# Performance work log

Hardware: AMD Instinct MI355X
Metric: run time of the kernel (lower is better)

The kernel has to match this reference:

```python
import jax, jax.numpy as jnp
import numpy as np
from jax import lax

C = 256
POOL = 7
NUM_CLASSES = 81
D = NUM_CLASSES - 1
STRIDES = (4, 8, 16, 32)
DEC_MULT = (0.1, 0.1, 0.2, 0.2)  # decode_settings: multipliers on raw deltas
LOG_MAX = float(np.log(1000.0 / 16.0))


def setup_inputs() -> dict:
    key = jax.random.key(0)
    ks = jax.random.split(key, 16)
    n, Rp = 2, 512
    R = n * Rp
    img = 800.0
    cx = jax.random.uniform(ks[0], (R,), minval=0.0, maxval=img)
    cy = jax.random.uniform(ks[1], (R,), minval=0.0, maxval=img)
    w = jax.random.uniform(ks[2], (R,), minval=16.0, maxval=300.0)
    h = jax.random.uniform(ks[3], (R,), minval=16.0, maxval=300.0)
    x1 = jnp.clip(cx - w / 2, 0.0, img - 1.0)
    y1 = jnp.clip(cy - h / 2, 0.0, img - 1.0)
    x2 = jnp.minimum(jnp.maximum(cx + w / 2, x1 + 1.0), img)
    y2 = jnp.minimum(jnp.maximum(cy + h / 2, y1 + 1.0), img)
    proposals = jnp.stack([x1, y1, x2, y2], -1)
    imidx = jnp.repeat(jnp.arange(n, dtype=jnp.int32), Rp)
    fmaps = {}
    for li, s in enumerate(STRIDES):
        hw = int(800 // s)
        fmaps[f"fmap{li}"] = jax.random.normal(ks[4 + li], (n, hw, hw, C), jnp.float32)
    c1, clin = C * POOL * POOL, 1024
    def lin(k, fi, fo):
        return (jax.random.normal(k, (fi, fo), jnp.float32) / np.sqrt(fi).astype(np.float32),
                jnp.zeros((fo,), jnp.float32))
    W0, b0 = lin(ks[8], c1, clin)
    W1, b1 = lin(ks[9], clin, clin)
    Wc, bc = lin(ks[10], clin, NUM_CLASSES)
    Wr, br = lin(ks[11], clin, NUM_CLASSES * 4)
    imsizes = jnp.full((n, 2), img, jnp.float32)  # (h, w) per image
    return dict(proposals=proposals, imidx=imidx, **fmaps,
                W0=W0, b0=b0, W1=W1, b1=b1, Wc=Wc, bc=bc, Wr=Wr, br=br,
                imsizes=imsizes, score_thr=0.05, iou_thr=0.5, imtop=100, min_size=1.0)


def _roi_align_level(fmap, boxes, imidx, stride):
    # fmap [n,H,W,C], boxes [R,4] xyxy in image coords; 1 sample per bin, bilinear.
    n, H, W, c = fmap.shape
    s = 1.0 / stride
    x1, y1, x2, y2 = boxes[:, 0] * s, boxes[:, 1] * s, boxes[:, 2] * s, boxes[:, 3] * s
    g = (jnp.arange(POOL, dtype=jnp.float32) + 0.5) / POOL  # bin centers in [0,1]
    xs = x1[:, None] + g[None, :] * (x2 - x1)[:, None] - 0.5  # [R,POOL]
    ys = y1[:, None] + g[None, :] * (y2 - y1)[:, None] - 0.5
    R = boxes.shape[0]
    xx = jnp.broadcast_to(xs[:, None, :], (R, POOL, POOL))
    yy = jnp.broadcast_to(ys[:, :, None], (R, POOL, POOL))
    x0f, y0f = jnp.floor(xx), jnp.floor(yy)
    wx, wy = xx - x0f, yy - y0f
    x0 = jnp.clip(x0f.astype(jnp.int32), 0, W - 1)
    x1i = jnp.clip(x0f.astype(jnp.int32) + 1, 0, W - 1)
    y0 = jnp.clip(y0f.astype(jnp.int32), 0, H - 1)
    y1i = jnp.clip(y0f.astype(jnp.int32) + 1, 0, H - 1)
    ii = imidx[:, None, None]
    v00 = fmap[ii, y0, x0]; v01 = fmap[ii, y0, x1i]
    v10 = fmap[ii, y1i, x0]; v11 = fmap[ii, y1i, x1i]  # each [R,POOL,POOL,C]
    wx, wy = wx[..., None], wy[..., None]
    return (v00 * (1 - wx) * (1 - wy) + v01 * wx * (1 - wy)
            + v10 * (1 - wx) * wy + v11 * wx * wy)


def _forward(proposals, imidx, fmaps, W0, b0, W1, b1, Wc, bc, Wr, br,
             imsizes, score_thr, iou_thr, imtop, min_size):
    R = proposals.shape[0]
    pw = proposals[:, 2] - proposals[:, 0]
    ph = proposals[:, 3] - proposals[:, 1]
    # FPN level assignment (torchvision canonical formula)
    lvl = jnp.floor(4.0 + jnp.log2(jnp.sqrt(pw * ph) / 224.0 + 1e-6))
    lvl = jnp.clip(lvl, 2, 5).astype(jnp.int32) - 2
    pooled = jnp.zeros((R, POOL, POOL, C), fmaps[0].dtype)
    for k, (fm, st) in enumerate(zip(fmaps, STRIDES)):
        pk = _roi_align_level(fm, proposals, imidx, st)
        pooled = jnp.where((lvl == k)[:, None, None, None], pk, pooled)
    # two-FC head + cls/reg
    x = pooled.reshape(R, -1)
    x = jax.nn.relu(x @ W0 + b0)
    x = jax.nn.relu(x @ W1 + b1)
    reg = (x @ Wr + br).reshape(R, NUM_CLASSES, 4)[:, 1:]      # [R,D,4]
    scr = jax.nn.softmax(x @ Wc + bc, axis=-1)[:, 1:]          # [R,D]
    cls = jnp.broadcast_to(jnp.arange(1, NUM_CLASSES, dtype=jnp.int32), (R, D))
    # decode boxes (proposal cwh + weighted deltas, log-space clamp)
    cx = (proposals[:, 0] + proposals[:, 2]) * 0.5
    cy = (proposals[:, 1] + proposals[:, 3]) * 0.5
    dx = reg[..., 0] * DEC_MULT[0]
    dy = reg[..., 1] * DEC_MULT[1]
    dw = jnp.minimum(reg[..., 2] * DEC_MULT[2], LOG_MAX)
    dh = jnp.minimum(reg[..., 3] * DEC_MULT[3], LOG_MAX)
    ncx = dx * pw[:, None] + cx[:, None]
    ncy = dy * ph[:, None] + cy[:, None]
    nw = jnp.exp(dw) * pw[:, None]
    nh = jnp.exp(dh) * ph[:, None]
    hb = imsizes[imidx, 0][:, None]
    wb = imsizes[imidx, 1][:, None]
    bx1 = jnp.clip(ncx - nw / 2, 0.0, wb); bx2 = jnp.clip(ncx + nw / 2, 0.0, wb)
    by1 = jnp.clip(ncy - nh / 2, 0.0, hb); by2 = jnp.clip(ncy + nh / 2, 0.0, hb)
    boxes = jnp.stack([bx1, by1, bx2, by2], -1)                # [R,D,4]
    valid = (scr > score_thr) & (bx2 - bx1 >= min_size) & (by2 - by1 >= min_size)
    # flatten roi-class pairs; class-offset boxes = torchvision batched_nms trick
    M = R * D
    boxes_f = boxes.reshape(M, 4)
    scr_f = scr.reshape(M)
    cls_f = cls.reshape(M)
    valid_f = valid.reshape(M)
    imidx_f = jnp.repeat(imidx, D)
    off = cls_f.astype(boxes_f.dtype)[:, None] * (jnp.max(imsizes) + 2.0)
    bo = boxes_f + off
    areas = (bo[:, 2] - bo[:, 0]) * (bo[:, 3] - bo[:, 1])
    def nms(scores0):
        def step(scores, _):
            i = jnp.argmax(scores)
            s = scores[i]
            b = bo[i]
            iw = jnp.clip(jnp.minimum(b[2], bo[:, 2]) - jnp.maximum(b[0], bo[:, 0]), 0.0)
            ih = jnp.clip(jnp.minimum(b[3], bo[:, 3]) - jnp.maximum(b[1], bo[:, 1]), 0.0)
            inter = iw * ih
            iou = inter / (areas[i] + areas - inter + 1e-6)
            scores = jnp.where(iou > iou_thr, -1.0, scores)
            scores = scores.at[i].set(-1.0)
            return scores, (i, s)
        _, (idx, s) = lax.scan(step, scores0, None, length=imtop)
        return idx, s
    n = imsizes.shape[0]
    ob, osc, ocl = [], [], []
    for i in range(n):
        s0 = jnp.where(valid_f & (imidx_f == i), scr_f, -1.0)
        idx, s = nms(s0)
        keep = s > 0.0  # padded slots have score <= 0
        ob.append(jnp.where(keep[:, None], boxes_f[idx], 0.0))
        osc.append(jnp.where(keep, s, 0.0))
        ocl.append(jnp.where(keep, cls_f[idx], -1))
    return jnp.stack(ob), jnp.stack(osc), jnp.stack(ocl)


def reference(proposals, imidx, fmap0, fmap1, fmap2, fmap3, W0, b0, W1, b1,
              Wc, bc, Wr, br, imsizes, score_thr, iou_thr, imtop, min_size):
    return _forward(proposals, imidx, (fmap0, fmap1, fmap2, fmap3), W0, b0, W1,
                    b1, Wc, bc, Wr, br, imsizes, score_thr, iou_thr, int(imtop),
                    min_size)
```

## Files before the change

### kernel.cpp

```cpp
#include <hip/hip_runtime.h>
#include <math.h>

#define CCH 256
#define NPOOL 7
#define NCLS 81
#define DCLS 80
#define NHEAD 512
#define FLOG_MAX 4.1351666f

typedef _Float16 half8 __attribute__((ext_vector_type(8)));
typedef _Float16 half4 __attribute__((ext_vector_type(4)));
typedef float floatx4 __attribute__((ext_vector_type(4)));

__global__ void zero_k(float4* __restrict__ p, int count4)
{
    int i = blockIdx.x * blockDim.x + threadIdx.x;
    if (i < count4) p[i] = make_float4(0.f, 0.f, 0.f, 0.f);
}

__device__ __forceinline__ void roi_setup(
    const float* __restrict__ prop, const int* __restrict__ imidx,
    const float* __restrict__ f0, const float* __restrict__ f1,
    const float* __restrict__ f2, const float* __restrict__ f3,
    int h0, int h1, int h2, int h3, int b,
// ... 9 lines not shown

    float lv = floorf(4.0f + log2f(sqrtf(pw * ph) / 224.0f + 1e-6f));
    lv = fminf(fmaxf(lv, 2.0f), 5.0f);
    int lvl = (int)lv - 2;

    const float* fm; int H; float s;
    if (lvl == 0)      { fm = f0; H = h0; s = 0.25f;    }
    else if (lvl == 1) { fm = f1; H = h1; s = 0.125f;   }
    else if (lvl == 2) { fm = f2; H = h2; s = 0.0625f;  }
    else               { fm = f3; H = h3; s = 0.03125f; }
    W = H;

    float xs1 = x1 * s, ys1 = y1 * s, xs2 = x2 * s, ys2 = y2 * s;
    float gx = (px + 0.5f) / 7.0f, gy = (py + 0.5f) / 7.0f;
    float xx = xs1 + gx * (xs2 - xs1) - 0.5f;
    float yy = ys1 + gy * (ys2 - ys1) - 0.5f;
    float x0f = floorf(xx), y0f = floorf(yy);
    float wx = xx - x0f, wy = yy - y0f;
    int x0i = min(max((int)x0f, 0), W - 1);
    int x1i = min(max((int)x0f + 1, 0), W - 1);
    int y0i = min(max((int)y0f, 0), H - 1);
    int y1i = min(max((int)y0f + 1, 0), H - 1);

    int ii = imidx[roi];
    base = fm + (size_t)ii * H * W * CCH;
    o00 = ((size_t)y0i * W + x0i) * CCH;
    o01 = ((size_t)y0i * W + x1i) * CCH;
    o10 = ((size_t)y1i * W + x0i) * CCH;
    o11 = ((size_t)y1i * W + x1i) * CCH;
    w00 = (1.0f - wx) * (1.0f - wy);
    w01 = wx * (1.0f - wy);
    w10 = (1.0f - wx) * wy;
    w11 = wx * wy;
}

__global__ void roi_align_k(const float* __restrict__ prop,
                            const int* __restrict__ imidx,
                            const float* __restrict__ f0,
                            const float* __restrict__ f1,
                            const float* __restrict__ f2,
                            const float* __restrict__ f3,
                            int h0, int h1, int h2, int h3,
                            float* __restrict__ pooled)
{
    int b = blockIdx.x, c = threadIdx.x;
    const float* base; int W; size_t o00, o01, o10, o11;
    float w00, w01, w10, w11;
    roi_setup(prop, imidx, f0, f1, f2, f3, h0, h1, h2, h3, b,
              base, W, o00, o01, o10, o11, w00, w01, w10, w11);
    float v = base[o00 + c] * w00 + base[o01 + c] * w01
            + base[o10 + c] * w10 + base[o11 + c] * w11;
    pooled[(size_t)b * CCH + c] = v;
}


__device__ __forceinline__ void roi_f16v4_body(
    const float* __restrict__ prop, const int* __restrict__ imidx,
    const float* __restrict__ f0, const float* __restrict__ f1,
    const float* __restrict__ f2, const float* __restrict__ f3,
    int h0, int h1, int h2, int h3, int bb, int t,
    _Float16* __restrict__ poolH, _Float16* __restrict__ poolL)
{
    int b = bb * 4 + (t >> 6);
    int lane = t & 63;
    const float* base; int W; size_t o00, o01, o10, o11;
    float w00, w01, w10, w11;
    roi_setup(prop, imidx, f0, f1, f2, f3, h0, h1, h2, h3, b,
              base, W, o00, o01, o10, o11, w00, w01, w10, w11);

    int c4 = lane * 4;
    float4 v00 = *(const float4*)(base + o00 + c4);
    float4 v01 = *(const float4*)(base + o01 + c4);
    float4 v10 = *(const float4*)(base + o10 + c4);
    float4 v11 = *(const float4*)(base + o11 + c4);
    const float* p00 = (const float*)&v00;
    const float* p01 = (const float*)&v01;
    const float* p10 = (const float*)&v10;
    const float* p11 = (const float*)&v11;

    half4 h, l;
#pragma unroll
    for (int e = 0; e < 4; ++e) {
        float v = p00[e] * w00 + p01[e] * w01 + p10[e] * w10 + p11[e] * w11;
        _Float16 hh = (_Float16)v;
        h[e] = hh;
        l[e] = (_Float16)(v - (float)hh);
    }
    size_t idx = (size_t)b * CCH + c4;
    *(half4*)(poolH + idx) = h;
    *(half4*)(poolL + idx) = l;
}

__device__ __forceinline__ void conv_fast_body(
    const float* __restrict__ W, _Float16* __restrict__ WtH,
    _Float16* __restrict__ WtL, int K, int N, int k0, int n0, int t,
    float (*sh)[65])
{
#pragma unroll
    for (int p = 0; p < 4; ++p) {
        int idx = p * 256 + t;
        int kr = idx >> 4, nc = (idx & 15) * 4;
        float4 v = *(const float4*)(W + (size_t)(k0 + kr) * N + n0 + nc);
        sh[kr][nc + 0] = v.x; sh[kr][nc + 1] = v.y;
        sh[kr][nc + 2] = v.z; sh[kr][nc + 3] = v.w;
    }
    __syncthreads();
#pragma unroll
// ... 9 lines not shown
            l[i] = (_Float16)(v - (float)hh);
        }
        *(half4*)(WtH + (size_t)(n0 + nr) * K + k0 + kc) = h;
        *(half4*)(WtL + (size_t)(n0 + nr) * K + k0 + kc) = l;
    }
}

__device__ __forceinline__ void conv_guard_body(
    const float* __restrict__ W, _Float16* __restrict__ WtH,
    _Float16* __restrict__ WtL, int K, int N, int Kt, int rowofs,
    int k0, int n0, int t, float (*sh)[65])
{
#pragma unroll
    for (int p = 0; p < 4; ++p) {
        int idx = p * 256 + t;
        int kr = idx >> 4, nc = (idx & 15) * 4;
#pragma unroll
        for (int e = 0; e < 4; ++e) {
            int nn = n0 + nc + e;
            sh[kr][nc + e] = (nn < N) ? W[(size_t)(k0 + kr) * N + nn] : 0.0f;
        }
    }
    __syncthreads();
#pragma unroll
    for (int p = 0; p < 4; ++p) {
        int idx = p * 256 + t;
        int nr = idx >> 4, kc = (idx & 15) * 4;
        if (n0 + nr < N) {
            half4 h, l;
#pragma unroll
            for (int i = 0; i < 4; ++i) {
                float v = sh[kc + i][nr];
                _Float16 hh = (_Float16)v;
                h[i] = hh;
                l[i] = (_Float16)(v - (float)hh);
            }
            *(half4*)(WtH + (size_t)(rowofs + n0 + nr) * Kt + k0 + kc) = h;
            *(half4*)(WtL + (size_t)(rowofs + n0 + nr) * Kt + k0 + kc) = l;
        }
    }
}

__global__ __launch_bounds__(256) void pre_uber_k(
    const float* __restrict__ prop, const int* __restrict__ imidx,
    const float* __restrict__ f0, const float* __restrict__ f1,
    const float* __restrict__ f2, const float* __restrict__ f3,
    int h0, int h1, int h2, int h3,
    _Float16* __restrict__ poolH, _Float16* __restrict__ poolL,
    const float* __restrict__ W0, _Float16* __restrict__ W0tH, _Float16* __restrict__ W0tL,
    const float* __restrict__ W1, _Float16* __restrict__ W1tH, _Float16* __restrict__ W1tL,
    const float* __restrict__ Wc, const float* __restrict__ Wr,
    _Float16* __restrict__ WheadtH, _Float16* __restrict__ WheadtL,
    float4* __restrict__ zp, int zc4,
    int R, int K0, int CL)
{
    __shared__ float sh[64][65];
    int b = blockIdx.x, t = threadIdx.x;

    int NB_ROI = (R * 49) / 4;
    int KT0 = K0 / 64, NT0 = CL / 64;
    int NB_CW0 = KT0 * NT0;
    int KT1 = CL / 64;
    int NB_CW1 = KT1 * KT1;
    int NTc = (NCLS + 63) / 64;
    int NB_CWc = KT1 * NTc;
    int NTr = (NCLS * 4 + 63) / 64;
    int NB_CWr = KT1 * NTr;

    if (b < NB_ROI) {
        roi_f16v4_body(prop, imidx, f0, f1, f2, f3, h0, h1, h2, h3, b, t,
                       poolH, poolL);
        return;
    }
    b -= NB_ROI;
    if (b < NB_CW0) {
        int k0 = (b % KT0) * 64, n0 = (b / KT0) * 64;
        conv_fast_body(W0, W0tH, W0tL, K0, CL, k0, n0, t, sh);
        return;
    }
    b -= NB_CW0;
    if (b < NB_CW1) {
        int k0 = (b % KT1) * 64, n0 = (b / KT1) * 64;
        conv_fast_body(W1, W1tH, W1tL, CL, CL, k0, n0, t, sh);
        return;
    }
    b -= NB_CW1;
    if (b < NB_CWc) {
        int k0 = (b % KT1) * 64, n0 = (b / KT1) * 64;
        conv_guard_body(Wc, WheadtH, WheadtL, CL, NCLS, CL, 0, k0, n0, t, sh);
        return;
    }
    b -= NB_CWc;
    if (b < NB_CWr) {
        int k0 = (b % KT1) * 64, n0 = (b / KT1) * 64;
        conv_guard_body(Wr, WheadtH, WheadtL, CL, NCLS * 4, CL, NCLS, k0, n0, t, sh);
        return;
    }
    b -= NB_CWr;
    {
        int i = b * 256 + t;
        if (i < zc4) zp[i] = make_float4(0.f, 0.f, 0.f, 0.f);
    }
}

__global__ __launch_bounds__(256) void convert_w_t_k(const float* __restrict__ W,
                                                     _Float16* __restrict__ WtH,
                                                     _Float16* __restrict__ WtL,
                                                     int K, int N)
{
    __shared__ float sh[64][65];
    conv_fast_body(W, WtH, WtL, K, N, blockIdx.x * 64, blockIdx.y * 64,
                   threadIdx.x, sh);
}

__global__ __launch_bounds__(256) void convert_w_t_guard_k(const float* __restrict__ W,
                                                           _Float16* __restrict__ WtH,
                                                           _Float16* __restrict__ WtL,
                                                           int K, int N, int Kt, int rowofs)
{
    __shared__ float sh[64][65];
    conv_guard_body(W, WtH, WtL, K, N, Kt, rowofs, blockIdx.x * 64,
                    blockIdx.y * 64, threadIdx.x, sh);
}

__global__ void act_split_k(const float* __restrict__ acc,
                            const float* __restrict__ bias,
                            _Float16* __restrict__ outH,
                            _Float16* __restrict__ outL,
                            int total, int CL)
{
    int i = (blockIdx.x * blockDim.x + threadIdx.x) * 4;
    if (i >= total) return;
    int b = i % CL;
    float4 v = *(const float4*)(acc + i);
    float4 bb = *(const float4*)(bias + b);
    const float* pv = (const float*)&v;
    const float* pb = (const float*)&bb;
    half4 h, l;
#pragma unroll
    for (int e = 0; e < 4; ++e) {
        float f = fmaxf(pv[e] + pb[e], 0.0f);
        _Float16 hh = (_Float16)f;
        h[e] = hh;
        l[e] = (_Float16)(f - (float)hh);
    }
    *(half4*)(outH + i) = h;
    *(half4*)(outL + i) = l;
}

__device__ __forceinline__ void dma16(const _Float16* g, _Float16* l)
{
    __builtin_amdgcn_global_load_lds(
        (const __attribute__((address_space(1))) unsigned int*)g,
        (__attribute__((address_space(3))) unsigned int*)l, 16, 0, 0);
}

#define LDKE 32
#define DKQ_SWZ(lane)  ((((lane) & 3) ^ (((lane) >> 3) & 3)) << 3)
#define FK_SWZ(lane)   (((((lane) >> 4) ^ (((lane) >> 1) & 3))) << 3)

__global__ __launch_bounds__(256) void gemm_mfma_split_k(
    const _Float16* __restrict__ Ah, const _Float16* __restrict__ Al,
    const _Float16* __restrict__ Bh, const _Float16* __restrict__ Bl,
    float* __restrict__ Cacc, int M, int N, int K, int Kc, int SP)
{
    __shared__ _Float16 sAh[128 * LDKE], sAl[128 * LDKE];
    __shared__ _Float16 sBh[128 * LDKE], sBl[128 * LDKE];

    int bid = blockIdx.x;
    int z = bid % SP;
    int q = bid / SP;
    int NT = N >> 7;
    int nn = q % NT;
    int m = q / NT;
    int m0 = m * 128, n0 = nn * 128;
    int kb = z * Kc;
    int ke = min(K, kb + Kc);

    int t = threadIdx.x;
    int lane = t & 63, w = t >> 6;
    int wr = w >> 1, wc = w & 1;
    int fr = lane & 15;
    int fk = FK_SWZ(lane);

    int drow = w * 32 + (lane >> 2);
    int dkq = DKQ_SWZ(lane);
    const _Float16* gAh = Ah + (size_t)(m0 + drow) * K + dkq;
    const _Float16* gAl = Al + (size_t)(m0 + drow) * K + dkq;
    const _Float16* gBh = Bh + (size_t)(n0 + drow) * K + dkq;
    const _Float16* gBl = Bl + (size_t)(n0 + drow) * K + dkq;
    size_t rowskip = (size_t)16 * K;

    _Float16* lAh0 = &sAh[(w * 2 + 0) * 512];
    _Float16* lAh1 = &sAh[(w * 2 + 1) * 512];
    _Float16* lAl0 = &sAl[(w * 2 + 0) * 512];
    _Float16* lAl1 = &sAl[(w * 2 + 1) * 512];
    _Float16* lBh0 = &sBh[(w * 2 + 0) * 512];
    _Float16* lBh1 = &sBh[(w * 2 + 1) * 512];
    _Float16* lBl0 = &sBl[(w * 2 + 0) * 512];
    _Float16* lBl1 = &sBl[(w * 2 + 1) * 512];

    floatx4 acc[4][4] = {};

    for (int k0 = kb; k0 < ke; k0 += 32) {
        dma16(gAh + k0, lAh0);
        dma16(gAh + rowskip + k0, lAh1);
        dma16(gAl + k0, lAl0);
        dma16(gAl + rowskip + k0, lAl1);
        dma16(gBh + k0, lBh0);
        dma16(gBh + rowskip + k0, lBh1);
        dma16(gBl + k0, lBl0);
        dma16(gBl + rowskip + k0, lBl1);
        __syncthreads();

        half8 ah[4], al[4], bh[4], bl[4];
#pragma unroll
        for (int i = 0; i < 4; ++i) {
            int ar = wr * 64 + i * 16 + fr;
            ah[i] = *(const half8*)&sAh[ar * LDKE + fk];
            al[i] = *(const half8*)&sAl[ar * LDKE + fk];
            int bc = wc * 64 + i * 16 + fr;
            bh[i] = *(const half8*)&sBh[bc * LDKE + fk];
            bl[i] = *(const half8*)&sBl[bc * LDKE + fk];
        }
#pragma unroll
        for (int i = 0; i < 4; ++i)
#pragma unroll
            for (int j = 0; j < 4; ++j) {
                acc[i][j] = __builtin_amdgcn_mfma_f32_16x16x32_f16(ah[i], bh[j], acc[i][j], 0, 0, 0);
                acc[i][j] = __builtin_amdgcn_mfma_f32_16x16x32_f16(ah[i], bl[j], acc[i][j], 0, 0, 0);
                acc[i][j] = __builtin_amdgcn_mfma_f32_16x16x32_f16(al[i], bh[j], acc[i][j], 0, 0, 0);
            }
        __syncthreads();
    }

    int rbase = (lane >> 4) * 4;
#pragma unroll
    for (int i = 0; i < 4; ++i)
#pragma unroll
        for (int j = 0; j < 4; ++j) {
            int col = n0 + wc * 64 + j * 16 + fr;
#pragma unroll
            for (int r = 0; r < 4; ++r) {
                int row = m0 + wr * 64 + i * 16 + rbase + r;
                atomicAdd(&Cacc[(size_t)row * N + col], acc[i][j][r]);
            }
        }
}

__global__ __launch_bounds__(256) void gemm_mfma_fused64_k(
    const _Float16* __restrict__ Ah, const _Float16* __restrict__ Al,
    const _Float16* __restrict__ Bh, const _Float16* __restrict__ Bl,
    const float* __restrict__ bias,
    float* __restrict__ Cout,
    _Float16* __restrict__ outH, _Float16* __restrict__ outL,
    int M, int N, int K, int mode)
{
    __shared__ _Float16 sAh[2][64 * LDKE], sAl[2][64 * LDKE];
    __shared__ _Float16 sBh[2][64 * LDKE], sBl[2][64 * LDKE];

    int m0 = blockIdx.y * 64, n0 = blockIdx.x * 64;
    int t = threadIdx.x;
    int lane = t & 63, w = t >> 6;
    int wr = w >> 1, wc = w & 1;
    int fr = lane & 15;
    int fk = FK_SWZ(lane);

    int drow = w * 16 + (lane >> 2);
    int dkq = DKQ_SWZ(lane);
    const _Float16* gAh = Ah + (size_t)(m0 + drow) * K + dkq;
    const _Float16* gAl = Al + (size_t)(m0 + drow) * K + dkq;
    const _Float16* gBh = Bh + (size_t)(n0 + drow) * K + dkq;
    const _Float16* gBl = Bl + (size_t)(n0 + drow) * K + dkq;
    int lofs = w * 512;

    int nt = K >> 5;

    dma16(gAh + 0, &sAh[0][lofs]);
    dma16(gAl + 0, &sAl[0][lofs]);
    dma16(gBh + 0, &sBh[0][lofs]);
    dma16(gBl + 0, &sBl[0][lofs]);
    __syncthreads();

    floatx4 acc[2][2] = {};

    for (int tt = 0; tt < nt; ++tt) {
        int c = tt & 1, nb = c ^ 1;
        if (tt + 1 < nt) {
            int k1 = (tt + 1) << 5;
            dma16(gAh + k1, &sAh[nb][lofs]);
            dma16(gAl + k1, &sAl[nb][lofs]);
            dma16(gBh + k1, &sBh[nb][lofs]);
            dma16(gBl + k1, &sBl[nb][lofs]);
        }
// ... 93 lines not shown

#pragma unroll
        for (int kk = 0; kk < 16; ++kk) {
            float4 af = *(const float4*)&Ast[kk][ty * 4];
            float4 bf = *(const float4*)&Bs[kk][tx * 4];
            float a_[4] = {af.x, af.y, af.z, af.w};
            float b_[4] = {bf.x, bf.y, bf.z, bf.w};
#pragma unroll
            for (int i = 0; i < 4; ++i)
#pragma unroll
                for (int j = 0; j < 4; ++j)
                    acc[i][j] = fmaf(a_[i], b_[j], acc[i][j]);
        }
    }

#pragma unroll
    for (int i = 0; i < 4; ++i) {
        int row = m0 + ty * 4 + i;
#pragma unroll
        for (int j = 0; j < 4; ++j) {
            int col = n0 + tx * 4 + j;
            if (col < N) atomicAdd(&Cacc[(size_t)row * N + col], acc[i][j]);
        }
    }
}

__global__ void softmax_k(const float* __restrict__ logits, int ldl,
                          const float* __restrict__ bc,
                          float* __restrict__ scr)
{
    int r = blockIdx.x;
    int t = threadIdx.x;
    const float* row = logits + (size_t)r * ldl;

    float v0 = row[t] + bc[t];
    float v1 = (t + 64 < NCLS) ? (row[t + 64] + bc[t + 64]) : -INFINITY;
    float m = fmaxf(v0, v1);
#pragma unroll
    for (int o = 32; o > 0; o >>= 1) m = fmaxf(m, __shfl_down(m, o));
    m = __shfl(m, 0);

    float e0 = expf(v0 - m);
    float e1 = (t + 64 < NCLS) ? expf(v1 - m) : 0.0f;
    float sum = e0 + e1;
#pragma unroll
    for (int o = 32; o > 0; o >>= 1) sum += __shfl_down(sum, o);
    sum = __shfl(sum, 0);
    float inv = 1.0f / sum;

    if (t >= 1)        scr[(size_t)r * DCLS + (t - 1)]  = e0 * inv;
    if (t + 64 < NCLS) scr[(size_t)r * DCLS + (t + 63)] = e1 * inv;
}

#define NMS_T 1024
#define NMS_SORTMAX 4096
#define NMS_AMAX 512
__global__ __launch_bounds__(NMS_T) void nms_k(
    const float* __restrict__ scr,
    const float* __restrict__ prop,
    const int* __restrict__ imidx,
    const float* __restrict__ head, int ldh, int regofs,
    const float* __restrict__ br,
    const float* __restrict__ imsz,
    const float* __restrict__ score_thr_p,
    const float* __restrict__ min_size_p,
    const float* __restrict__ iou_thr_p,
    int* __restrict__ cidx,
    float* __restrict__ cscore,
    float* __restrict__ cbo,
    float* __restrict__ cbox,
    float* __restrict__ carea,
    float* __restrict__ out,
    int M, int n, int imtop)
{
    int img = blockIdx.x;
    int t = threadIdx.x;
    const int T = NMS_T;
    const int NW = NMS_T / 64;
    int lane = t & 63, wid = t >> 6;

    __shared__ int cnt;
    __shared__ unsigned long long skey[NMS_SORTMAX];
    __shared__ int sp_[NMS_SORTMAX];
    __shared__ float aab0[NMS_AMAX], aab1[NMS_AMAX], aab2[NMS_AMAX], aab3[NMS_AMAX], aaa[NMS_AMAX];
    __shared__ int f_it;
    __shared__ float ws_sc[NW];
    __shared__ int ws_g[NW], ws_p[NW];
    __shared__ float f_sc, f_o0, f_o1, f_o2, f_o3, f_ar;

    if (t == 0) cnt = 0;
    __syncthreads();

    float score_thr = score_thr_p[0];
    float min_size  = min_size_p[0];
    float iou_thr   = iou_thr_p[0];
    float immax = imsz[0];
    for (int q = 1; q < 2 * n; ++q) immax = fmaxf(immax, imsz[q]);

    int base = img * M;
    for (int j = t; j < M; j += T) {
        int r = j / DCLS;
        if (imidx[r] != img) continue;
        float s = scr[j];
        if (s <= score_thr) continue;

        int cls = j - r * DCLS + 1;
        const float* pr = prop + (size_t)r * 4;
        float pw = pr[2] - pr[0], ph = pr[3] - pr[1];
        float cx = (pr[0] + pr[2]) * 0.5f, cy = (pr[1] + pr[3]) * 0.5f;
        const float* rg_ = head + (size_t)r * ldh + regofs + cls * 4;
        const float* bb = br + cls * 4;
        float dx = (rg_[0] + bb[0]) * 0.1f;
        float dy = (rg_[1] + bb[1]) * 0.1f;
        float dw = fminf((rg_[2] + bb[2]) * 0.2f, FLOG_MAX);
        float dh = fminf((rg_[3] + bb[3]) * 0.2f, FLOG_MAX);
        float ncx = dx * pw + cx;
        float ncy = dy * ph + cy;
        float nw = expf(dw) * pw;
        float nh = expf(dh) * ph;
        float hbound = imsz[img * 2 + 0];
        float wbound = imsz[img * 2 + 1];
        float bx1 = fminf(fmaxf(ncx - nw * 0.5f, 0.0f), wbound);
        float bx2 = fminf(fmaxf(ncx + nw * 0.5f, 0.0f), wbound);
        float by1 = fminf(fmaxf(ncy - nh * 0.5f, 0.0f), hbound);
        float by2 = fminf(fmaxf(ncy + nh * 0.5f, 0.0f), hbound);
        if (bx2 - bx1 < min_size || by2 - by1 < min_size) continue;

        float off = (float)cls * (immax + 2.0f);
        int p = atomicAdd(&cnt, 1);
        cidx[base + p] = j;
        cscore[base + p] = s;
        cbox[(size_t)(base + p) * 4 + 0] = bx1;
        cbox[(size_t)(base + p) * 4 + 1] = by1;
        cbox[(size_t)(base + p) * 4 + 2] = bx2;
        cbox[(size_t)(base + p) * 4 + 3] = by2;
        cbo[(size_t)(base + p) * 4 + 0] = bx1 + off;
        cbo[(size_t)(base + p) * 4 + 1] = by1 + off;
        cbo[(size_t)(base + p) * 4 + 2] = bx2 + off;
        cbo[(size_t)(base + p) * 4 + 3] = by2 + off;
        carea[base + p] = (bx2 - bx1) * (by2 - by1);
    }
    __syncthreads();
    int K = cnt;

    float* ob  = out;
    float* osc = out + (size_t)n * imtop * 4;
    float* ocl = out + (size_t)n * imtop * 5;

    int it = 0;
    if (K <= NMS_SORTMAX && imtop <= NMS_AMAX) {
        int SN = 64; while (SN < K) SN <<= 1;
        for (int i = t; i < SN; i += T) {
            if (i < K) {
                unsigned int sb = __float_as_uint(cscore[base + i]);
                skey[i] = ((unsigned long long)sb << 32)
                        | (unsigned int)(~cidx[base + i]);
            } else {
                skey[i] = 0ull;
            }
            sp_[i] = i;
        }
        for (int k = 2; k <= SN; k <<= 1) {
            for (int j = k >> 1; j > 0; j >>= 1) {
                __syncthreads();
                for (int i = t; i < SN; i += T) {
                    int l = i ^ j;
                    if (l > i) {
                        unsigned long long ki = skey[i], kl = skey[l];
                        bool up = ((i & k) == 0);
                        bool sw = up ? (ki < kl) : (ki > kl);
                        if (sw) {
                            skey[i] = kl; skey[l] = ki;
                            int tp = sp_[i]; sp_[i] = sp_[l]; sp_[l] = tp;
                        }
                    }
                }
            }
        }
        __syncthreads();

        if (wid == 0) {
            int na = 0;
            for (int c0 = 0; c0 < K && na < imtop; c0 += 64) {
                int ci = c0 + lane;
                bool alive = ci < K;
                float x0 = 0.f, x1 = 0.f, x2 = 0.f, x3 = 0.f, ar_ = 0.f, sc = 0.f;
                float q0 = 0.f, q1 = 0.f, q2 = 0.f, q3 = 0.f;
                int g = 0;
                if (alive) {
                    unsigned long long key = skey[ci];
                    sc = __uint_as_float((unsigned int)(key >> 32));
                    int pp = sp_[ci];
                    g = cidx[base + pp];
                    x0 = cbo[(size_t)(base + pp) * 4 + 0];
                    x1 = cbo[(size_t)(base + pp) * 4 + 1];
                    x2 = cbo[(size_t)(base + pp) * 4 + 2];
// ... 73 lines not shown
                    int   ol = __shfl_down(l2, o);
                    if (os > b2 || (os == b2 && og < g2)) { b2 = os; g2 = og; l2 = ol; }
                }
                if (lane == 0) {
                    f_sc = b2;
                    if (b2 > 0.0f) {
                        int lp = l2;
                        size_t oslot = (size_t)img * imtop + it;
                        ob[oslot * 4 + 0] = cbox[(size_t)(base + lp) * 4 + 0];
                        ob[oslot * 4 + 1] = cbox[(size_t)(base + lp) * 4 + 1];
                        ob[oslot * 4 + 2] = cbox[(size_t)(base + lp) * 4 + 2];
                        ob[oslot * 4 + 3] = cbox[(size_t)(base + lp) * 4 + 3];
                        osc[oslot] = b2;
                        ocl[oslot] = (float)(g2 % DCLS + 1);
                        f_o0 = cbo[(size_t)(base + lp) * 4 + 0];
                        f_o1 = cbo[(size_t)(base + lp) * 4 + 1];
                        f_o2 = cbo[(size_t)(base + lp) * 4 + 2];
                        f_o3 = cbo[(size_t)(base + lp) * 4 + 3];
                        f_ar = carea[base + lp];
                        cscore[base + lp] = -1.0f;
                    }
                }
            }
            __syncthreads();
            if (f_sc <= 0.0f) break;

            float b0 = f_o0, b1 = f_o1, b2_ = f_o2, b3 = f_o3, ai = f_ar;
            for (int p = t; p < K; p += T) {
                float c0 = cbo[(size_t)(base + p) * 4 + 0];
                float c1 = cbo[(size_t)(base + p) * 4 + 1];
                float c2 = cbo[(size_t)(base + p) * 4 + 2];
                float c3 = cbo[(size_t)(base + p) * 4 + 3];
                float iw = fmaxf(fminf(b2_, c2) - fmaxf(b0, c0), 0.0f);
                float ih = fmaxf(fminf(b3, c3) - fmaxf(b1, c1), 0.0f);
                float inter = iw * ih;
                float iou = inter / (ai + carea[base + p] - inter + 1e-6f);
                if (iou > iou_thr) cscore[base + p] = -1.0f;
            }
            __syncthreads();
        }
    }

    for (int q = it + t; q < imtop; q += T) {
        size_t oslot = (size_t)img * imtop + q;
        ob[oslot * 4 + 0] = 0.0f;
        ob[oslot * 4 + 1] = 0.0f;
        ob[oslot * 4 + 2] = 0.0f;
        ob[oslot * 4 + 3] = 0.0f;
        osc[oslot] = 0.0f;
        ocl[oslot] = -1.0f;
    }
}

extern "C" void kernel_launch(void* const* d_in, const int* in_sizes, int n_in,
                              void* d_out, int out_size, void* d_ws, size_t ws_size,
                              hipStream_t stream)
{
    const float* prop   = (const float*)d_in[0];
    const int*   imidx  = (const int*)d_in[1];
    const float* f0     = (const float*)d_in[2];
    const float* f1     = (const float*)d_in[3];
    const float* f2     = (const float*)d_in[4];
    const float* f3     = (const float*)d_in[5];
    const float* W0     = (const float*)d_in[6];
    const float* b0     = (const float*)d_in[7];
    const float* W1     = (const float*)d_in[8];
    const float* b1     = (const float*)d_in[9];
    const float* Wc     = (const float*)d_in[10];
    const float* bc     = (const float*)d_in[11];
    const float* Wr     = (const float*)d_in[12];
    const float* br     = (const float*)d_in[13];
    const float* imsz   = (const float*)d_in[14];
    const float* sthr   = (const float*)d_in[15];
    const float* ithr   = (const float*)d_in[16];
    const float* msz    = (const float*)d_in[18];

    int R = in_sizes[1];
    int n = in_sizes[14] / 2;
    int imtop = out_size / (n * 6);
    int M = R * DCLS;
    int K0 = NPOOL * NPOOL * CCH;
    int CL = in_sizes[7];

    int h0 = (int)(sqrtf((float)(in_sizes[2] / (n * CCH))) + 0.5f);
    int h1 = (int)(sqrtf((float)(in_sizes[3] / (n * CCH))) + 0.5f);
    int h2 = (int)(sqrtf((float)(in_sizes[4] / (n * CCH))) + 0.5f);
    int h3 = (int)(sqrtf((float)(in_sizes[5] / (n * CCH))) + 0.5f);

    float* outf = (float*)d_out;

    size_t szPool  = (size_t)R * K0 * 2;
    size_t szX     = (size_t)R * CL * 4;
    size_t szHead  = (size_t)R * NHEAD * 4;
    size_t szWh    = (size_t)NHEAD * CL * 2;
    size_t szXh    = (size_t)R * CL * 2;
    size_t szW1t   = (size_t)CL * CL * 2;
    size_t szScr   = (size_t)R * DCLS * 4;

    size_t needed = 4 * szPool + 2 * szX + szHead + 2 * szWh
                  + 4 * szXh + 2 * szW1t + szScr;

    int splitK0 = 8;
    bool mfma_ok = (ws_size >= needed) && (R % 128 == 0) && (CL % 128 == 0)
                 && (K0 % (splitK0 * 32) == 0) && (CL % 32 == 0)
                 && ((R * 49) % 4 == 0) && (K0 % 64 == 0) && (CL % 64 == 0);

    if (mfma_ok) {
        uint8_t* w = (uint8_t*)d_ws;
        size_t o = 0;
        _Float16* poolH   = (_Float16*)(w + o); o += szPool;
        _Float16* poolL   = (_Float16*)(w + o); o += szPool;
        _Float16* W0tH    = (_Float16*)(w + o); o += szPool;
        _Float16* W0tL    = (_Float16*)(w + o); o += szPool;
        float*    x0acc   = (float*)(w + o);    o += szX;
        float*    unused  = (float*)(w + o);    o += szX;
        float*    headacc = (float*)(w + o);    o += szHead;
        _Float16* WheadtH = (_Float16*)(w + o); o += szWh;
        _Float16* WheadtL = (_Float16*)(w + o); o += szWh;
        _Float16* x0H     = (_Float16*)(w + o); o += szXh;
        _Float16* x0L     = (_Float16*)(w + o); o += szXh;
        _Float16* x1H     = (_Float16*)(w + o); o += szXh;
        _Float16* x1L     = (_Float16*)(w + o); o += szXh;
        _Float16* W1tH    = (_Float16*)(w + o); o += szW1t;
        _Float16* W1tL    = (_Float16*)(w + o); o += szW1t;
        float*    scr     = (float*)(w + o);
        (void)unused;

        int*   cidx   = (int*)d_ws;
        float* cscore = (float*)(cidx + (size_t)n * M);
        float* cbo    = cscore + (size_t)n * M;
        float* cbox   = cbo + (size_t)n * M * 4;
        float* carea  = cbox + (size_t)n * M * 4;

        {
            int NB_ROI = (R * 49) / 4;
            int NB_CW0 = (K0 / 64) * (CL / 64);
            int NB_CW1 = (CL / 64) * (CL / 64);
            int NB_CWc = (CL / 64) * ((NCLS + 63) / 64);
            int NB_CWr = (CL / 64) * ((NCLS * 4 + 63) / 64);
            int zc4    = (int)(szX / 16);
            int NB_Z   = (zc4 + 255) / 256;
            int NB = NB_ROI + NB_CW0 + NB_CW1 + NB_CWc + NB_CWr + NB_Z;
            pre_uber_k<<<dim3(NB), dim3(256), 0, stream>>>(
                prop, imidx, f0, f1, f2, f3, h0, h1, h2, h3,
                poolH, poolL,
                W0, W0tH, W0tL,
                W1, W1tH, W1tL,
                Wc, Wr, WheadtH, WheadtL,
                (float4*)x0acc, zc4,
                R, K0, CL);
        }
        gemm_mfma_split_k<<<dim3(splitK0 * (R / 128) * (CL / 128)), dim3(256), 0, stream>>>(
            poolH, poolL, W0tH, W0tL, x0acc, R, CL, K0, K0 / splitK0, splitK0);
        act_split_k<<<dim3((R * CL / 4 + 255) / 256), dim3(256), 0, stream>>>(
            x0acc, b0, x0H, x0L, R * CL, CL);
        gemm_mfma_fused64_k<<<dim3(CL / 64, R / 64), dim3(256), 0, stream>>>(
            x0H, x0L, W1tH, W1tL, b1, nullptr, x1H, x1L, R, CL, CL, 1);
        gemm_mfma_fused64_k<<<dim3(NHEAD / 64, R / 64), dim3(256), 0, stream>>>(
            x1H, x1L, WheadtH, WheadtL, nullptr, headacc, nullptr, nullptr, R, NHEAD, CL, 0);
        softmax_k<<<dim3(R), dim3(64), 0, stream>>>(headacc, NHEAD, bc, scr);
        nms_k<<<dim3(n), dim3(NMS_T), 0, stream>>>(
            scr, prop, imidx, headacc, NHEAD, NCLS, br, imsz, sthr, msz, ithr,
            cidx, cscore, cbo, cbox, carea, outf, M, n, imtop);
    } else {
        float* ws = (float*)d_ws;
        size_t off = 0;
        float* pooled  = ws + off; off += (size_t)R * K0;
        float* x0acc   = ws + off; off += (size_t)R * CL;
        float* x1acc   = ws + off; off += (size_t)R * CL;
        float* logits  = ws + off; off += (size_t)R * NCLS;
        off = (off + 3) & ~(size_t)3;
        float* reg     = ws + off; off += (size_t)R * NCLS * 4;
        float* scr     = ws + off; off += (size_t)R * DCLS;

        int*   cidx   = (int*)ws;
        float* cscore = (float*)(cidx + (size_t)n * M);
        float* cbo    = cscore + (size_t)n * M;
        float* cbox   = cbo + (size_t)n * M * 4;
        float* carea  = cbox + (size_t)n * M * 4;

        {
            size_t zcount = (size_t)(reg + (size_t)R * NCLS * 4 - x0acc);
            int c4 = (int)(zcount / 4);
            zero_k<<<dim3((c4 + 255) / 256), dim3(256), 0, stream>>>((float4*)x0acc, c4);
        }
        roi_align_k<<<dim3(R * 49), dim3(256), 0, stream>>>(
            prop, imidx, f0, f1, f2, f3, h0, h1, h2, h3, pooled);
        gemm_splitk_k<<<dim3(CL / 64, R / 64, 8), dim3(256), 0, stream>>>(
            pooled, W0, nullptr, x0acc, R, CL, K0, 1568);
        gemm_splitk_k<<<dim3(CL / 64, R / 64, 4), dim3(256), 0, stream>>>(
            x0acc, W1, b0, x1acc, R, CL, CL, 256);
        gemm_splitk_k<<<dim3((NCLS + 63) / 64, R / 64, 8), dim3(256), 0, stream>>>(
            x1acc, Wc, b1, logits, R, NCLS, CL, 128);
        gemm_splitk_k<<<dim3((NCLS * 4 + 63) / 64, R / 64, 4), dim3(256), 0, stream>>>(
            x1acc, Wr, b1, reg, R, NCLS * 4, CL, 256);
        softmax_k<<<dim3(R), dim3(64), 0, stream>>>(logits, NCLS, bc, scr);
        nms_k<<<dim3(n), dim3(NMS_T), 0, stream>>>(
            scr, prop, imidx, reg, NCLS * 4, 0, br, imsz, sthr, msz, ithr,
            cidx, cscore, cbo, cbox, carea, outf, M, n, imtop);
    }
}
```

Before: 401.9 us.

## Split NMS compaction into parallel kernel fused with softmax; narrow split-K GEMM tile

```diff
diff --git a/kernel.cpp b/kernel.cpp
--- a/kernel.cpp
+++ b/kernel.cpp
@@ -85,7 +85,6 @@
             + base[o10 + c] * w10 + base[o11 + c] * w11;
     pooled[(size_t)b * CCH + c] = v;
 }
-
 
 __device__ __forceinline__ void roi_f16v4_body(
     const float* __restrict__ prop, const int* __restrict__ imidx,
@@ -201,10 +200,13 @@
     const float* __restrict__ Wc, const float* __restrict__ Wr,
     _Float16* __restrict__ WheadtH, _Float16* __restrict__ WheadtL,
     float4* __restrict__ zp, int zc4,
+    int* __restrict__ cntp, int ncnt,
     int R, int K0, int CL)
 {
     __shared__ float sh[64][65];
     int b = blockIdx.x, t = threadIdx.x;
+
+    if (blockIdx.x == 0 && t < ncnt) cntp[t] = 0;
 
     int NB_ROI = (R * 49) / 4;
     int KT0 = K0 / 64, NT0 = CL / 64;
@@ -252,26 +254,6 @@
     }
 }
 
-__global__ __launch_bounds__(256) void convert_w_t_k(const float* __restrict__ W,
-                                                     _Float16* __restrict__ WtH,
-                                                     _Float16* __restrict__ WtL,
-                                                     int K, int N)
-{
-    __shared__ float sh[64][65];
-    conv_fast_body(W, WtH, WtL, K, N, blockIdx.x * 64, blockIdx.y * 64,
-                   threadIdx.x, sh);
-}
-
-__global__ __launch_bounds__(256) void convert_w_t_guard_k(const float* __restrict__ W,
-                                                           _Float16* __restrict__ WtH,
-                                                           _Float16* __restrict__ WtL,
-                                                           int K, int N, int Kt, int rowofs)
-{
-    __shared__ float sh[64][65];
-    conv_guard_body(W, WtH, WtL, K, N, Kt, rowofs, blockIdx.x * 64,
-                    blockIdx.y * 64, threadIdx.x, sh);
-}
-
 __global__ void act_split_k(const float* __restrict__ acc,
                             const float* __restrict__ bias,
                             _Float16* __restrict__ outH,
@@ -314,15 +296,15 @@
     float* __restrict__ Cacc, int M, int N, int K, int Kc, int SP)
 {
     __shared__ _Float16 sAh[128 * LDKE], sAl[128 * LDKE];
-    __shared__ _Float16 sBh[128 * LDKE], sBl[128 * LDKE];
+    __shared__ _Float16 sBh[64 * LDKE],  sBl[64 * LDKE];
 
     int bid = blockIdx.x;
     int z = bid % SP;
     int q = bid / SP;
-    int NT = N >> 7;
+    int NT = N >> 6;
     int nn = q % NT;
     int m = q / NT;
-    int m0 = m * 128, n0 = nn * 128;
+    int m0 = m * 128, n0 = nn * 64;
     int kb = z * Kc;
     int ke = min(K, kb + Kc);
 
@@ -332,50 +314,50 @@
     int fr = lane & 15;
     int fk = FK_SWZ(lane);
 
-    int drow = w * 32 + (lane >> 2);
+    int drowA = w * 32 + (lane >> 2);
+    int drowB = w * 16 + (lane >> 2);
     int dkq = DKQ_SWZ(lane);
-    const _Float16* gAh = Ah + (size_t)(m0 + drow) * K + dkq;
-    const _Float16* gAl = Al + (size_t)(m0 + drow) * K + dkq;
-    const _Float16* gBh = Bh + (size_t)(n0 + drow) * K + dkq;
-    const _Float16* gBl = Bl + (size_t)(n0 + drow) * K + dkq;
+    const _Float16* gAh = Ah + (size_t)(m0 + drowA) * K + dkq;
+    const _Float16* gAl = Al + (size_t)(m0 + drowA) * K + dkq;
+    const _Float16* gBh = Bh + (size_t)(n0 + drowB) * K + dkq;
+    const _Float16* gBl = Bl + (size_t)(n0 + drowB) * K + dkq;
     size_t rowskip = (size_t)16 * K;
 
     _Float16* lAh0 = &sAh[(w * 2 + 0) * 512];
     _Float16* lAh1 = &sAh[(w * 2 + 1) * 512];
     _Float16* lAl0 = &sAl[(w * 2 + 0) * 512];
     _Float16* lAl1 = &sAl[(w * 2 + 1) * 512];
-    _Float16* lBh0 = &sBh[(w * 2 + 0) * 512];
-    _Float16* lBh1 = &sBh[(w * 2 + 1) * 512];
-    _Float16* lBl0 = &sBl[(w * 2 + 0) * 512];
-    _Float16* lBl1 = &sBl[(w * 2 + 1) * 512];
-
-    floatx4 acc[4][4] = {};
+    _Float16* lBh  = &sBh[w * 512];
+    _Float16* lBl  = &sBl[w * 512];
+
+    floatx4 acc[4][2] = {};
 
     for (int k0 = kb; k0 < ke; k0 += 32) {
         dma16(gAh + k0, lAh0);
         dma16(gAh + rowskip + k0, lAh1);
         dma16(gAl + k0, lAl0);
         dma16(gAl + rowskip + k0, lAl1);
-        dma16(gBh + k0, lBh0);
-        dma16(gBh + rowskip + k0, lBh1);
-        dma16(gBl + k0, lBl0);
-        dma16(gBl + rowskip + k0, lBl1);
+        dma16(gBh + k0, lBh);
+        dma16(gBl + k0, lBl);
         __syncthreads();
 
-        half8 ah[4], al[4], bh[4], bl[4];
+        half8 ah[4], al[4], bh[2], bl[2];
 #pragma unroll
         for (int i = 0; i < 4; ++i) {
             int ar = wr * 64 + i * 16 + fr;
             ah[i] = *(const half8*)&sAh[ar * LDKE + fk];
             al[i] = *(const half8*)&sAl[ar * LDKE + fk];
-            int bc = wc * 64 + i * 16 + fr;
-            bh[i] = *(const half8*)&sBh[bc * LDKE + fk];
-            bl[i] = *(const half8*)&sBl[bc * LDKE + fk];
+        }
+#pragma unroll
+        for (int j = 0; j < 2; ++j) {
+            int bcc = wc * 32 + j * 16 + fr;
+            bh[j] = *(const half8*)&sBh[bcc * LDKE + fk];
+            bl[j] = *(const half8*)&sBl[bcc * LDKE + fk];
         }
 #pragma unroll
         for (int i = 0; i < 4; ++i)
 #pragma unroll
-            for (int j = 0; j < 4; ++j) {
+            for (int j = 0; j < 2; ++j) {
                 acc[i][j] = __builtin_amdgcn_mfma_f32_16x16x32_f16(ah[i], bh[j], acc[i][j], 0, 0, 0);
                 acc[i][j] = __builtin_amdgcn_mfma_f32_16x16x32_f16(ah[i], bl[j], acc[i][j], 0, 0, 0);
                 acc[i][j] = __builtin_amdgcn_mfma_f32_16x16x32_f16(al[i], bh[j], acc[i][j], 0, 0, 0);
@@ -387,8 +369,8 @@
 #pragma unroll
     for (int i = 0; i < 4; ++i)
 #pragma unroll
-        for (int j = 0; j < 4; ++j) {
-            int col = n0 + wc * 64 + j * 16 + fr;
+        for (int j = 0; j < 2; ++j) {
+            int col = n0 + wc * 32 + j * 16 + fr;
 #pragma unroll
             for (int r = 0; r < 4; ++r) {
                 int row = m0 + wr * 64 + i * 16 + rbase + r;
@@ -588,62 +570,63 @@
     if (t + 64 < NCLS) scr[(size_t)r * DCLS + (t + 63)] = e1 * inv;
 }
 
-#define NMS_T 1024
-#define NMS_SORTMAX 4096
-#define NMS_AMAX 512
-__global__ __launch_bounds__(NMS_T) void nms_k(
-    const float* __restrict__ scr,
+__global__ __launch_bounds__(256) void compact_k(
+    const float* __restrict__ head, int ldh, int regofs,
+    const float* __restrict__ bc,
+    const float* __restrict__ br,
     const float* __restrict__ prop,
     const int* __restrict__ imidx,
-    const float* __restrict__ head, int ldh, int regofs,
-    const float* __restrict__ br,
     const float* __restrict__ imsz,
     const float* __restrict__ score_thr_p,
     const float* __restrict__ min_size_p,
-    const float* __restrict__ iou_thr_p,
+    int* __restrict__ cntp,
     int* __restrict__ cidx,
     float* __restrict__ cscore,
     float* __restrict__ cbo,
     float* __restrict__ cbox,
     float* __restrict__ carea,
-    float* __restrict__ out,
-    int M, int n, int imtop)
-{
-    int img = blockIdx.x;
-    int t = threadIdx.x;
-    const int T = NMS_T;
-    const int NW = NMS_T / 64;
-    int lane = t & 63, wid = t >> 6;
-
-    __shared__ int cnt;
-    __shared__ unsigned long long skey[NMS_SORTMAX];
-    __shared__ int sp_[NMS_SORTMAX];
-    __shared__ float aab0[NMS_AMAX], aab1[NMS_AMAX], aab2[NMS_AMAX], aab3[NMS_AMAX], aaa[NMS_AMAX];
-    __shared__ int f_it;
-    __shared__ float ws_sc[NW];
-    __shared__ int ws_g[NW], ws_p[NW];
-    __shared__ float f_sc, f_o0, f_o1, f_o2, f_o3, f_ar;
-
-    if (t == 0) cnt = 0;
-    __syncthreads();
+    int M, int n, int R)
+{
+    int wid = threadIdx.x >> 6, t = threadIdx.x & 63;
+    int r = blockIdx.x * 4 + wid;
+    if (r >= R) return;
+
+    const float* row = head + (size_t)r * ldh;
+    float v0 = row[t] + bc[t];
+    float v1 = (t + 64 < NCLS) ? (row[t + 64] + bc[t + 64]) : -INFINITY;
+    float m = fmaxf(v0, v1);
+#pragma unroll
+    for (int o = 32; o > 0; o >>= 1) m = fmaxf(m, __shfl_down(m, o));
+    m = __shfl(m, 0);
+
+    float e0 = expf(v0 - m);
+    float e1 = (t + 64 < NCLS) ? expf(v1 - m) : 0.0f;
+    float sum = e0 + e1;
+#pragma unroll
+    for (int o = 32; o > 0; o >>= 1) sum += __shfl_down(sum, o);
+    sum = __shfl(sum, 0);
+    float inv = 1.0f / sum;
 
     float score_thr = score_thr_p[0];
     float min_size  = min_size_p[0];
-    float iou_thr   = iou_thr_p[0];
     float immax = imsz[0];
     for (int q = 1; q < 2 * n; ++q) immax = fmaxf(immax, imsz[q]);
 
+    int img = imidx[r];
     int base = img * M;
-    for (int j = t; j < M; j += T) {
-        int r = j / DCLS;
-        if (imidx[r] != img) continue;
-        float s = scr[j];
-        if (s <= score_thr) continue;
-
-        int cls = j - r * DCLS + 1;
-        const float* pr = prop + (size_t)r * 4;
-        float pw = pr[2] - pr[0], ph = pr[3] - pr[1];
-        float cx = (pr[0] + pr[2]) * 0.5f, cy = (pr[1] + pr[3]) * 0.5f;
+    const float* pr = prop + (size_t)r * 4;
+    float pw = pr[2] - pr[0], ph = pr[3] - pr[1];
+    float cx = (pr[0] + pr[2]) * 0.5f, cy = (pr[1] + pr[3]) * 0.5f;
+    float hbound = imsz[img * 2 + 0];
+    float wbound = imsz[img * 2 + 1];
+
+#pragma unroll
+    for (int pass = 0; pass < 2; ++pass) {
+        int cls; float s; bool active;
+        if (pass == 0) { cls = t;      s = e0 * inv; active = (t >= 1); }
+        else           { cls = t + 64; s = e1 * inv; active = (t + 64 < NCLS); }
+        if (!active || s <= score_thr) continue;
+
         const float* rg_ = head + (size_t)r * ldh + regofs + cls * 4;
         const float* bb = br + cls * 4;
         float dx = (rg_[0] + bb[0]) * 0.1f;
@@ -654,8 +637,6 @@
         float ncy = dy * ph + cy;
         float nw = expf(dw) * pw;
         float nh = expf(dh) * ph;
-        float hbound = imsz[img * 2 + 0];
-        float wbound = imsz[img * 2 + 1];
         float bx1 = fminf(fmaxf(ncx - nw * 0.5f, 0.0f), wbound);
         float bx2 = fminf(fmaxf(ncx + nw * 0.5f, 0.0f), wbound);
         float by1 = fminf(fmaxf(ncy - nh * 0.5f, 0.0f), hbound);
@@ -663,7 +644,8 @@
         if (bx2 - bx1 < min_size || by2 - by1 < min_size) continue;
 
         float off = (float)cls * (immax + 2.0f);
-        int p = atomicAdd(&cnt, 1);
+        int j = r * DCLS + cls - 1;
+        int p = atomicAdd(&cntp[img], 1);
         cidx[base + p] = j;
         cscore[base + p] = s;
         cbox[(size_t)(base + p) * 4 + 0] = bx1;
@@ -676,8 +658,39 @@
         cbo[(size_t)(base + p) * 4 + 3] = by2 + off;
         carea[base + p] = (bx2 - bx1) * (by2 - by1);
     }
-    __syncthreads();
-    int K = cnt;
+}
+
+#define NMS_T 1024
+#define NMS_SORTMAX 4096
+#define NMS_AMAX 512
+__global__ __launch_bounds__(NMS_T) void nms_pick_k(
+    const float* __restrict__ iou_thr_p,
+    const int* __restrict__ cntp,
+    int* __restrict__ cidx,
+    float* __restrict__ cscore,
+    float* __restrict__ cbo,
+    float* __restrict__ cbox,
+    float* __restrict__ carea,
+    float* __restrict__ out,
+    int M, int n, int imtop)
+{
+    int img = blockIdx.x;
+    int t = threadIdx.x;
+    const int T = NMS_T;
+    const int NW = NMS_T / 64;
+    int lane = t & 63, wid = t >> 6;
+
+    __shared__ unsigned long long skey[NMS_SORTMAX];
+    __shared__ int sp_[NMS_SORTMAX];
+    __shared__ float aab0[NMS_AMAX], aab1[NMS_AMAX], aab2[NMS_AMAX], aab3[NMS_AMAX], aaa[NMS_AMAX];
+    __shared__ int f_it;
+    __shared__ float ws_sc[NW];
+    __shared__ int ws_g[NW], ws_p[NW];
+    __shared__ float f_sc, f_o0, f_o1, f_o2, f_o3, f_ar;
+
+    float iou_thr = iou_thr_p[0];
+    int K = cntp[img];
+    int base = img * M;
 
     float* ob  = out;
     float* osc = out + (size_t)n * imtop * 4;
@@ -857,6 +870,171 @@
     }
 }
 
+__global__ __launch_bounds__(NMS_T) void nms_k(
+    const float* __restrict__ scr,
+    const float* __restrict__ prop,
+    const int* __restrict__ imidx,
+    const float* __restrict__ head, int ldh, int regofs,
+    const float* __restrict__ br,
+    const float* __restrict__ imsz,
+    const float* __restrict__ score_thr_p,
+    const float* __restrict__ min_size_p,
+    const float* __restrict__ iou_thr_p,
+    int* __restrict__ cidx,
+    float* __restrict__ cscore,
+    float* __restrict__ cbo,
+    float* __restrict__ cbox,
+    float* __restrict__ carea,
+    float* __restrict__ out,
+    int M, int n, int imtop)
+{
+    int img = blockIdx.x;
+    int t = threadIdx.x;
+    const int T = NMS_T;
+    const int NW = NMS_T / 64;
+    int lane = t & 63, wid = t >> 6;
+
+    __shared__ int cnt;
+    __shared__ float ws_sc[NW];
+    __shared__ int ws_g[NW], ws_p[NW];
+    __shared__ float f_sc, f_o0, f_o1, f_o2, f_o3, f_ar;
+
+    if (t == 0) cnt = 0;
+    __syncthreads();
+
+    float score_thr = score_thr_p[0];
+    float min_size  = min_size_p[0];
+    float iou_thr   = iou_thr_p[0];
+    float immax = imsz[0];
+    for (int q = 1; q < 2 * n; ++q) immax = fmaxf(immax, imsz[q]);
+
+    int base = img * M;
+    for (int j = t; j < M; j += T) {
+        int r = j / DCLS;
+        if (imidx[r] != img) continue;
+        float s = scr[j];
+        if (s <= score_thr) continue;
+
+        int cls = j - r * DCLS + 1;
+        const float* pr = prop + (size_t)r * 4;
+        float pw = pr[2] - pr[0], ph = pr[3] - pr[1];
+        float cx = (pr[0] + pr[2]) * 0.5f, cy = (pr[1] + pr[3]) * 0.5f;
+        const float* rg_ = head + (size_t)r * ldh + regofs + cls * 4;
+        const float* bb = br + cls * 4;
+        float dx = (rg_[0] + bb[0]) * 0.1f;
+        float dy = (rg_[1] + bb[1]) * 0.1f;
+        float dw = fminf((rg_[2] + bb[2]) * 0.2f, FLOG_MAX);
+        float dh = fminf((rg_[3] + bb[3]) * 0.2f, FLOG_MAX);
+        float ncx = dx * pw + cx;
+        float ncy = dy * ph + cy;
+        float nw = expf(dw) * pw;
+        float nh = expf(dh) * ph;
+        float hbound = imsz[img * 2 + 0];
+        float wbound = imsz[img * 2 + 1];
+        float bx1 = fminf(fmaxf(ncx - nw * 0.5f, 0.0f), wbound);
+        float bx2 = fminf(fmaxf(ncx + nw * 0.5f, 0.0f), wbound);
+        float by1 = fminf(fmaxf(ncy - nh * 0.5f, 0.0f), hbound);
+        float by2 = fminf(fmaxf(ncy + nh * 0.5f, 0.0f), hbound);
+        if (bx2 - bx1 < min_size || by2 - by1 < min_size) continue;
+
+        float off = (float)cls * (immax + 2.0f);
+        int p = atomicAdd(&cnt, 1);
+        cidx[base + p] = j;
+        cscore[base + p] = s;
+        cbox[(size_t)(base + p) * 4 + 0] = bx1;
+        cbox[(size_t)(base + p) * 4 + 1] = by1;
+        cbox[(size_t)(base + p) * 4 + 2] = bx2;
+        cbox[(size_t)(base + p) * 4 + 3] = by2;
+        cbo[(size_t)(base + p) * 4 + 0] = bx1 + off;
+        cbo[(size_t)(base + p) * 4 + 1] = by1 + off;
+        cbo[(size_t)(base + p) * 4 + 2] = bx2 + off;
+        cbo[(size_t)(base + p) * 4 + 3] = by2 + off;
+        carea[base + p] = (bx2 - bx1) * (by2 - by1);
+    }
+    __syncthreads();
+    int K = cnt;
+
+    float* ob  = out;
+    float* osc = out + (size_t)n * imtop * 4;
+    float* ocl = out + (size_t)n * imtop * 5;
+
+    int it = 0;
+    for (; it < imtop; ++it) {
+        float best = -1e30f; int bg = 0x7fffffff; int bl = -1;
+        for (int p = t; p < K; p += T) {
+            float sv = cscore[base + p];
+            int g = cidx[base + p];
+            if (sv > best || (sv == best && g < bg)) { best = sv; bg = g; bl = p; }
+        }
+#pragma unroll
+        for (int o = 32; o > 0; o >>= 1) {
+            float os = __shfl_down(best, o);
+            int   og = __shfl_down(bg, o);
+            int   ol = __shfl_down(bl, o);
+            if (os > best || (os == best && og < bg)) { best = os; bg = og; bl = ol; }
+        }
+        if (lane == 0) { ws_sc[wid] = best; ws_g[wid] = bg; ws_p[wid] = bl; }
+        __syncthreads();
+        if (wid == 0) {
+            float b2 = (lane < NW) ? ws_sc[lane] : -1e30f;
+            int   g2 = (lane < NW) ? ws_g[lane] : 0x7fffffff;
+            int   l2 = (lane < NW) ? ws_p[lane] : -1;
+#pragma unroll
+            for (int o = NW / 2; o > 0; o >>= 1) {
+                float os = __shfl_down(b2, o);
+                int   og = __shfl_down(g2, o);
+                int   ol = __shfl_down(l2, o);
+                if (os > b2 || (os == b2 && og < g2)) { b2 = os; g2 = og; l2 = ol; }
+            }
+            if (lane == 0) {
+                f_sc = b2;
+                if (b2 > 0.0f) {
+                    int lp = l2;
+                    size_t oslot = (size_t)img * imtop + it;
+                    ob[oslot * 4 + 0] = cbox[(size_t)(base + lp) * 4 + 0];
+                    ob[oslot * 4 + 1] = cbox[(size_t)(base + lp) * 4 + 1];
+                    ob[oslot * 4 + 2] = cbox[(size_t)(base + lp) * 4 + 2];
+                    ob[oslot * 4 + 3] = cbox[(size_t)(base + lp) * 4 + 3];
+                    osc[oslot] = b2;
+                    ocl[oslot] = (float)(g2 % DCLS + 1);
+                    f_o0 = cbo[(size_t)(base + lp) * 4 + 0];
+                    f_o1 = cbo[(size_t)(base + lp) * 4 + 1];
+                    f_o2 = cbo[(size_t)(base + lp) * 4 + 2];
+                    f_o3 = cbo[(size_t)(base + lp) * 4 + 3];
+                    f_ar = carea[base + lp];
+                    cscore[base + lp] = -1.0f;
+                }
+            }
+        }
+        __syncthreads();
+        if (f_sc <= 0.0f) break;
+
+        float b0 = f_o0, b1 = f_o1, b2_ = f_o2, b3 = f_o3, ai = f_ar;
+        for (int p = t; p < K; p += T) {
+            float c0 = cbo[(size_t)(base + p) * 4 + 0];
+            float c1 = cbo[(size_t)(base + p) * 4 + 1];
+            float c2 = cbo[(size_t)(base + p) * 4 + 2];
+            float c3 = cbo[(size_t)(base + p) * 4 + 3];
+            float iw = fmaxf(fminf(b2_, c2) - fmaxf(b0, c0), 0.0f);
+            float ih = fmaxf(fminf(b3, c3) - fmaxf(b1, c1), 0.0f);
+            float inter = iw * ih;
+            float iou = inter / (ai + carea[base + p] - inter + 1e-6f);
+            if (iou > iou_thr) cscore[base + p] = -1.0f;
+        }
+        __syncthreads();
+    }
+
+    for (int q = it + t; q < imtop; q += T) {
+        size_t oslot = (size_t)img * imtop + q;
+        ob[oslot * 4 + 0] = 0.0f;
+        ob[oslot * 4 + 1] = 0.0f;
+        ob[oslot * 4 + 2] = 0.0f;
+        ob[oslot * 4 + 3] = 0.0f;
+        osc[oslot] = 0.0f;
+        ocl[oslot] = -1.0f;
+    }
+}
+
 extern "C" void kernel_launch(void* const* d_in, const int* in_sizes, int n_in,
                               void* d_out, int out_size, void* d_ws, size_t ws_size,
                               hipStream_t stream)
@@ -908,7 +1086,8 @@
     int splitK0 = 8;
     bool mfma_ok = (ws_size >= needed) && (R % 128 == 0) && (CL % 128 == 0)
                  && (K0 % (splitK0 * 32) == 0) && (CL % 32 == 0)
-                 && ((R * 49) % 4 == 0) && (K0 % 64 == 0) && (CL % 64 == 0);
+                 && ((R * 49) % 4 == 0) && (K0 % 64 == 0) && (CL % 64 == 0)
+                 && (R % 4 == 0);
 
     if (mfma_ok) {
         uint8_t* w = (uint8_t*)d_ws;
@@ -931,6 +1110,8 @@
         float*    scr     = (float*)(w + o);
         (void)unused;
 
+        int* cnt = (int*)scr;
+
         int*   cidx   = (int*)d_ws;
         float* cscore = (float*)(cidx + (size_t)n * M);
         float* cbo    = cscore + (size_t)n * M;
@@ -953,9 +1134,10 @@
                 W1, W1tH, W1tL,
                 Wc, Wr, WheadtH, WheadtL,
                 (float4*)x0acc, zc4,
+                cnt, n,
                 R, K0, CL);
         }
-        gemm_mfma_split_k<<<dim3(splitK0 * (R / 128) * (CL / 128)), dim3(256), 0, stream>>>(
+        gemm_mfma_split_k<<<dim3(splitK0 * (R / 128) * (CL / 64)), dim3(256), 0, stream>>>(
             poolH, poolL, W0tH, W0tL, x0acc, R, CL, K0, K0 / splitK0, splitK0);
         act_split_k<<<dim3((R * CL / 4 + 255) / 256), dim3(256), 0, stream>>>(
             x0acc, b0, x0H, x0L, R * CL, CL);
@@ -963,10 +1145,11 @@
             x0H, x0L, W1tH, W1tL, b1, nullptr, x1H, x1L, R, CL, CL, 1);
         gemm_mfma_fused64_k<<<dim3(NHEAD / 64, R / 64), dim3(256), 0, stream>>>(
             x1H, x1L, WheadtH, WheadtL, nullptr, headacc, nullptr, nullptr, R, NHEAD, CL, 0);
-        softmax_k<<<dim3(R), dim3(64), 0, stream>>>(headacc, NHEAD, bc, scr);
-        nms_k<<<dim3(n), dim3(NMS_T), 0, stream>>>(
-            scr, prop, imidx, headacc, NHEAD, NCLS, br, imsz, sthr, msz, ithr,
-            cidx, cscore, cbo, cbox, carea, outf, M, n, imtop);
+        compact_k<<<dim3(R / 4), dim3(256), 0, stream>>>(
+            headacc, NHEAD, NCLS, bc, br, prop, imidx, imsz, sthr, msz,
+            cnt, cidx, cscore, cbo, cbox, carea, M, n, R);
+        nms_pick_k<<<dim3(n), dim3(NMS_T), 0, stream>>>(
+            ithr, cnt, cidx, cscore, cbo, cbox, carea, outf, M, n, imtop);
     } else {
         float* ws = (float*)d_ws;
         size_t off = 0;
```

Result: faster. 385.2 us (-4.2%).
